# Optimization experiments

Measured on AMD Instinct MI355X. Metric: run time of the kernel, lower is better.

## Reference

```python
import jax, jax.numpy as jnp
import numpy as np

B, C, L, D, H = 8, 64, 256, 64, 4
HD = C // H  # head_dim = 16
EPS = 1e-5


def _conv(x, w):
    # x: [B,C,L,D], w: [O,I,kh,kw], stride 1, SAME padding (matches padding=1 for 3x3, 0 for 1x1)
    return jax.lax.conv_general_dilated(
        x, w, window_strides=(1, 1), padding='SAME',
        dimension_numbers=('NCHW', 'OIHW', 'NCHW'))


def setup_inputs() -> dict:
    rng = jax.random.key(0)
    ks = jax.random.split(rng, 10)
    n = lambda k, s: jax.random.normal(k, s, dtype=jnp.float32)
    xav3 = float(np.sqrt(6.0 / (C * 9 + C * 9)))  # xavier_uniform bound for 3x3 conv
    xav1 = float(np.sqrt(6.0 / (C + C)))
    u = lambda k, s, b: jax.random.uniform(k, s, jnp.float32, -b, b)
    return {
        'query': n(ks[0], (B, C, L, D)),
        'key': n(ks[1], (B, C, L, D)),
        'value': n(ks[2], (B, C, L, D)),
        'Wq': u(ks[3], (C, C, 3, 3), xav3),
        'Wk': u(ks[4], (C, C, 3, 3), xav3),
        'Wv': u(ks[5], (C, C, 3, 3), xav3),
        'Wo': u(ks[6], (C, C, 1, 1), xav1),
        'bo': jnp.zeros((C,), jnp.float32),
        'gamma': jnp.ones((C,), jnp.float32),
        'beta': jnp.zeros((C,), jnp.float32),
    }


def reference(query, key, value, Wq, Wk, Wv, Wo, bo, gamma, beta):
    identity = query
    # projections -> [B, H, HD, L, D]
    Q = _conv(query, Wq).reshape(B, H, HD, L, D)
    K = _conv(key, Wk).reshape(B, H, HD, L, D)
    V = _conv(value, Wv).reshape(B, H, HD, L, D)
    # attention over L, contraction over D; head_dim acts as an extra batch dim
    scores = jnp.einsum('bhcld,bhcmd->bhclm', Q, K) / jnp.sqrt(jnp.float32(HD))
    attn = jax.nn.softmax(scores, axis=-1)  # dropout is identity in eval mode
    out = jnp.einsum('bhclm,bhcmd->bhcld', attn, V).reshape(B, C, L, D)
    out = _conv(out, Wo) + bo[None, :, None, None] + identity
    # LayerNorm over channel dim (original permutes C last)
    mu = jnp.mean(out, axis=1, keepdims=True)
    var = jnp.var(out, axis=1, keepdims=True)
    out = (out - mu) * jax.lax.rsqrt(var + EPS)
    out = out * gamma[None, :, None, None] + beta[None, :, None, None]
    return out
```

## Files before the change

kernel.cpp:

```cpp
#include <hip/hip_runtime.h>

typedef _Float16 f16;
typedef f16   f16x8 __attribute__((ext_vector_type(8)));
typedef float f32x4 __attribute__((ext_vector_type(4)));

#define MFMA(a,b,c) __builtin_amdgcn_mfma_f32_16x16x32_f16(a,b,c,0,0,0)

__device__ __forceinline__ f32x4 fz4(){ f32x4 z; z[0]=0.f; z[1]=0.f; z[2]=0.f; z[3]=0.f; return z; }
__device__ __forceinline__ f16x8 hz8(){ f16x8 z;
#pragma unroll
  for(int i=0;i<8;++i) z[i]=(f16)0.f;
  return z; }

#define NBLK 256u

__device__ __forceinline__ void grid_barrier(unsigned* bar) {
  __syncthreads();
  if (threadIdx.x == 0) {
    __threadfence();
    unsigned gen  = atomicAdd(&bar[1], 0u);
    unsigned prev = atomicAdd(&bar[0], 1u);
    if (prev == NBLK - 1u) {
      atomicExch(&bar[0], 0u);
      __threadfence();
      atomicAdd(&bar[1], 1u);
    } else {
      while (atomicAdd(&bar[1], 0u) == gen) __builtin_amdgcn_s_sleep(2);
    }
    __threadfence();
  }
  __syncthreads();
}

__global__ __launch_bounds__(512, 2) void mega(
    const float* __restrict__ query, const float* __restrict__ key,
    const float* __restrict__ value,
    const float* __restrict__ Wq, const float* __restrict__ Wk,
    const float* __restrict__ Wv, const float* __restrict__ Wo,
    const float* __restrict__ bo, const float* __restrict__ gamma,
    const float* __restrict__ beta,
    f16* __restrict__ QKV, f16* __restrict__ AO,
    f16* WA, float* out, unsigned* bar)
{
  __shared__ f16 smem[32768];
  const int tid  = threadIdx.x;
  const int bid  = blockIdx.x;
  const int half = tid >> 8;
  const int ltid = tid & 255;
  const int lane = tid & 63;
  const int wvg  = tid >> 6;
  const int wvl  = (ltid >> 6);
  const int lr   = lane & 15, kh = lane >> 4;
  f16* hs = smem + half*16384;

  {
    int gid = bid*512 + tid;
    if (gid < 110592) {
      int t = gid / 36864, r = gid % 36864;
      const float* W = (t==0)?Wq:((t==1)?Wk:Wv);
      float sc = (t==0) ? 0.25f : 1.0f;
      int kstep = r >> 11, rem = r & 2047;
      int co = rem >> 5, rem2 = rem & 31;
      int kq = rem2 >> 3, j = rem2 & 7;
      int k = kstep*32 + kq*8 + j;
      int sp = k >> 6, ci = k & 63;
      int ky = sp/3, kx = sp - ky*3;
      WA[gid] = (f16)(W[((co*64+ci)*3+ky)*3+kx]*sc);
    }
  }
  grid_barrier(bar);

  for (int iter = 0; iter < 6; ++iter) {
    int w    = bid + (iter*2 + half)*256;
    int b    = w & 7;
    int rest = w >> 3;
    int t    = rest >> 7;
    int l0   = (rest & 127) * 2;
    const float* X = (t==0)?query:((t==1)?key:value);
    const f16* WAt = WA + t*36864;
    f16* Yt = QKV + (size_t)t*8388608;
    {
      int ci0 = (ltid & 31)*2;
      int row = (ltid >> 5) & 3;
      int dh  = (ltid >> 7) * 32;
      int gr  = l0 - 1 + row;
      bool valid = (unsigned)gr < 256u;
      int grc = valid ? gr : 0;
      const f32x4* s0 = (const f32x4*)(X + (((size_t)(b*64+ci0  )*256 + grc)*64 + dh));
      const f32x4* s1 = (const f32x4*)(X + (((size_t)(b*64+ci0+1)*256 + grc)*64 + dh));
#pragma unroll
      for (int q=0;q<8;++q) {
        f32x4 f0 = valid ? s0[q] : fz4();
        f32x4 f1 = valid ? s1[q] : fz4();
#pragma unroll
        for (int e=0;e<4;++e) {
          int d = dh + q*4 + e;
          int idx = ((row*64 + d)*64 + ci0) ^ ((d&7)<<3);
          unsigned int pk = (unsigned int)__builtin_bit_cast(unsigned short,(f16)f0[e])
                          | ((unsigned int)__builtin_bit_cast(unsigned short,(f16)f1[e]) << 16);
          *(unsigned int*)&hs[idx] = pk;
        }
      }
    }
    __syncthreads();
    f32x4 acc[4][2];
#pragma unroll
    for (int mt=0;mt<4;++mt){ acc[mt][0]=fz4(); acc[mt][1]=fz4(); }
    for (int kstep=0; kstep<18; ++kstep) {
      int sp = kstep >> 1;
      int sp3 = sp/3;
      int dl = sp3 - 1;
      int dd = (sp - sp3*3) - 1;
      int cib = (kstep & 1)*32;
      const f16* wp = WAt + kstep*2048 + lr*32 + kh*8;
      f16x8 a0 = *(const f16x8*)(wp);
      f16x8 a1 = *(const f16x8*)(wp + 512);
      f16x8 a2 = *(const f16x8*)(wp + 1024);
      f16x8 a3 = *(const f16x8*)(wp + 1536);
      f16x8 bb[2];
#pragma unroll
      for (int nt=0;nt<2;++nt) {
        int n = wvl*32 + nt*16 + lr;
        int lloc = n >> 6, d = n & 63;
        int dp = d + dd;
        bool v = (unsigned)dp < 64u;
        int dpc = dp & 63;
        int rowi = lloc + dl + 1;
        int idx = ((rowi*64 + dpc)*64 + cib + kh*8) ^ ((dpc&7)<<3);
        f16x8 tt = *(const f16x8*)&hs[idx];
        if (!v) tt = hz8();
        bb[nt] = tt;
      }
#pragma unroll
      for (int nt=0;nt<2;++nt) {
        acc[0][nt] = MFMA(a0, bb[nt], acc[0][nt]);
        acc[1][nt] = MFMA(a1, bb[nt], acc[1][nt]);
        acc[2][nt] = MFMA(a2, bb[nt], acc[2][nt]);
        acc[3][nt] = MFMA(a3, bb[nt], acc[3][nt]);
      }
    }
#pragma unroll
    for (int mt=0;mt<4;++mt)
#pragma unroll
    for (int nt=0;nt<2;++nt)
#pragma unroll
    for (int r=0;r<4;++r) {
      int co = mt*16 + kh*4 + r;
      int n = wvl*32 + nt*16 + lr;
      int lrow = l0 + (n>>6), d = n & 63;
      Yt[((size_t)(b*64+co)*256 + lrow)*64 + d] = (f16)acc[mt][nt][r];
    }
    __syncthreads();
  }
  grid_barrier(bar);

  for (int k2 = 0; k2 < 2; ++k2) {
    int idx = bid + k2*256;
    int bc = (idx & 7)*64 + (idx >> 3);
    const f16* Qs = QKV + (size_t)bc*16384;
    const f16* Ks = QKV +  8388608 + (size_t)bc*16384;
    const f16* Vs = QKV + 16777216 + (size_t)bc*16384;
    __syncthreads();
    {
      int m  = tid & 63;
      int dg = (tid >> 6) * 8;
#pragma unroll
      for (int pass=0; pass<4; ++pass) {
        int mm = m + pass*64;
        f16x8 v0 = *(const f16x8*)(Vs + mm*64 + dg);
#pragma unroll
        for (int e=0;e<8;++e){ int d=dg+e; smem[(d*256+mm) ^ ((d&7)<<3)] = v0[e]; }
      }
    }
    int l0g = wvg*32;
    f16x8 qf[2][2];
#pragma unroll
    for (int lt=0;lt<2;++lt)
#pragma unroll
    for (int ks=0;ks<2;++ks)
      qf[lt][ks] = *(const f16x8*)(Qs + (l0g + lt*16 + lr)*64 + ks*32 + kh*8);
    f32x4 O[2][4];
    float rm[2][4], rl[2][4];
#pragma unroll
    for (int lt=0;lt<2;++lt)
#pragma unroll
    for (int x=0;x<4;++x) { O[lt][x]=fz4(); rm[lt][x]=-1e30f; rl[lt][x]=0.f; }
    __syncthreads();
    f16* P = &smem[16384 + wvg*2048];
    for (int it=0; it<4; ++it) {
      int m0 = it*64;
      f32x4 s[2][4];
#pragma unroll
      for (int lt=0;lt<2;++lt)
#pragma unroll
      for (int mt=0;mt<4;++mt) s[lt][mt]=fz4();
#pragma unroll
      for (int ks=0;ks<2;++ks) {
        f16x8 kf[4];
#pragma unroll
        for (int mt=0;mt<4;++mt)
          kf[mt] = *(const f16x8*)(Ks + (m0 + mt*16 + lr)*64 + ks*32 + kh*8);
#pragma unroll
        for (int lt=0;lt<2;++lt)
#pragma unroll
        for (int mt=0;mt<4;++mt)
          s[lt][mt] = MFMA(qf[lt][ks], kf[mt], s[lt][mt]);
      }
#pragma unroll
      for (int lt=0;lt<2;++lt)
#pragma unroll
      for (int r=0;r<4;++r) {
        float tm = fmaxf(fmaxf(s[lt][0][r], s[lt][1][r]), fmaxf(s[lt][2][r], s[lt][3][r]));
#pragma unroll
        for (int off=1; off<16; off<<=1) tm = fmaxf(tm, __shfl_xor(tm, off));
        float mo = rm[lt][r];
        float mn = fmaxf(mo, tm);
        rm[lt][r] = mn;
        float corr = __expf(mo - mn);
        float sum = 0.f;
#pragma unroll
        for (int mt=0;mt<4;++mt) { float p = __expf(s[lt][mt][r] - mn); s[lt][mt][r] = p; sum += p; }
#pragma unroll
        for (int off=1; off<16; off<<=1) sum += __shfl_xor(sum, off);
        rl[lt][r] = rl[lt][r]*corr + sum;
#pragma unroll
        for (int dt=0;dt<4;++dt) O[lt][dt][r] *= corr;
      }
#pragma unroll
      for (int lt=0;lt<2;++lt)
#pragma unroll
      for (int mt=0;mt<4;++mt)
#pragma unroll
      for (int r=0;r<4;++r) {
        int row = lt*16 + kh*4 + r;
        P[(row*64 + mt*16 + lr) ^ ((row&7)<<3)] = (f16)s[lt][mt][r];
      }
#pragma unroll
      for (int ks=0;ks<2;++ks) {
        f16x8 pa[2], vb[4];
#pragma unroll
        for (int lt=0;lt<2;++lt) {
          int row = lt*16 + lr;
          pa[lt] = *(const f16x8*)&P[(row*64 + ks*32 + kh*8) ^ ((row&7)<<3)];
        }
#pragma unroll
        for (int dt=0;dt<4;++dt) {
          int d = dt*16 + lr;
          vb[dt] = *(const f16x8*)&smem[(d*256 + m0 + ks*32 + kh*8) ^ ((d&7)<<3)];
        }
#pragma unroll
        for (int lt=0;lt<2;++lt)
#pragma unroll
        for (int dt=0;dt<4;++dt)
          O[lt][dt] = MFMA(pa[lt], vb[dt], O[lt][dt]);
      }
    }
#pragma unroll
    for (int lt=0;lt<2;++lt)
#pragma unroll
    for (int r=0;r<4;++r) {
      float inv = 1.f / rl[lt][r];
      int row = l0g + lt*16 + kh*4 + r;
#pragma unroll
      for (int dt=0;dt<4;++dt)
        AO[(size_t)bc*16384 + row*64 + dt*16 + lr] = (f16)(O[lt][dt][r]*inv);
    }
  }
  grid_barrier(bar);

  for (int iter = 0; iter < 2; ++iter) {
    int w  = bid + (iter*2 + half)*256;
    int b  = w & 7;
    int p0 = (w >> 3) * 128;
    {
      int ci = ltid & 63;
      int pg = ltid >> 6;
      const f16* src = AO + (size_t)(b*64+ci)*16384 + p0 + pg*32;
      f16x8 v[4];
#pragma unroll
      for (int q=0;q<4;++q) v[q] = *(const f16x8*)(src + q*8);
#pragma unroll
      for (int q=0;q<4;++q)
#pragma unroll
      for (int e=0;e<8;++e) {
        int p = pg*32 + q*8 + e;
        hs[(p*64 + ci) ^ ((p&7)<<3)] = v[q][e];
      }
      int co  = ltid >> 2;
      int cig = (ltid & 3) * 16;
      const f32x4* wsrc = (const f32x4*)(Wo + co*64 + cig);
      f32x4 w0 = wsrc[0], w1 = wsrc[1], w2 = wsrc[2], w3 = wsrc[3];
      f16x8 g0, g1;
#pragma unroll
      for (int e=0;e<4;++e) { g0[e]=(f16)w0[e]; g0[4+e]=(f16)w1[e]; g1[e]=(f16)w2[e]; g1[4+e]=(f16)w3[e]; }
      *(f16x8*)&hs[8192 + ((co*64 + cig    ) ^ ((co&7)<<3))] = g0;
      *(f16x8*)&hs[8192 + ((co*64 + cig + 8) ^ ((co&7)<<3))] = g1;
    }
    __syncthreads();
    int n0 = wvl*32;
    f32x4 acc[4][2];
#pragma unroll
    for (int mt=0;mt<4;++mt){ acc[mt][0]=fz4(); acc[mt][1]=fz4(); }
#pragma unroll
    for (int ks=0;ks<2;++ks) {
      f16x8 a[4], bb[2];
#pragma unroll
      for (int mt=0;mt<4;++mt)
        a[mt] = *(const f16x8*)&hs[8192 + (((mt*16+lr)*64 + ks*32 + kh*8) ^ ((lr&7)<<3))];
#pragma unroll
      for (int nt=0;nt<2;++nt) {
        int p = n0 + nt*16 + lr;
        bb[nt] = *(const f16x8*)&hs[(p*64 + ks*32 + kh*8) ^ ((p&7)<<3)];
      }
#pragma unroll
      for (int mt=0;mt<4;++mt)
#pragma unroll
      for (int nt=0;nt<2;++nt)
        acc[mt][nt] = MFMA(a[mt], bb[nt], acc[mt][nt]);
    }
    float vals[4][2][4];
    float sum0=0.f, sq0=0.f, sum1=0.f, sq1=0.f;
#pragma unroll
    for (int mt=0;mt<4;++mt)
#pragma unroll
    for (int nt=0;nt<2;++nt)
#pragma unroll
    for (int r=0;r<4;++r) {
      int co = mt*16 + kh*4 + r;
      int p  = p0 + n0 + nt*16 + lr;
      float v = acc[mt][nt][r] + bo[co] + query[(size_t)(b*64+co)*16384 + p];
      vals[mt][nt][r] = v;
      if (nt==0) { sum0 += v; sq0 += v*v; } else { sum1 += v; sq1 += v*v; }
    }
#pragma unroll
    for (int off=16; off<64; off<<=1) {
      sum0 += __shfl_xor(sum0, off); sq0 += __shfl_xor(sq0, off);
      sum1 += __shfl_xor(sum1, off); sq1 += __shfl_xor(sq1, off);
    }
    float mu0 = sum0*(1.f/64.f), var0 = sq0*(1.f/64.f) - mu0*mu0, rs0 = rsqrtf(var0 + 1e-5f);
    float mu1 = sum1*(1.f/64.f), var1 = sq1*(1.f/64.f) - mu1*mu1, rs1 = rsqrtf(var1 + 1e-5f);
#pragma unroll
    for (int mt=0;mt<4;++mt)
#pragma unroll
    for (int nt=0;nt<2;++nt)
#pragma unroll
    for (int r=0;r<4;++r) {
      int co = mt*16 + kh*4 + r;
      int p  = p0 + n0 + nt*16 + lr;
      float mu = nt ? mu1 : mu0;
      float rs = nt ? rs1 : rs0;
      out[(size_t)(b*64+co)*16384 + p] = (vals[mt][nt][r] - mu)*rs*gamma[co] + beta[co];
    }
    __syncthreads();
  }
}

extern "C" void kernel_launch(void* const* d_in, const int* in_sizes, int n_in,
                              void* d_out, int out_size, void* d_ws, size_t ws_size,
                              hipStream_t stream)
{
  const float* query = (const float*)d_in[0];
  const float* key   = (const float*)d_in[1];
  const float* value = (const float*)d_in[2];
  const float* Wq = (const float*)d_in[3];
  const float* Wk = (const float*)d_in[4];
  const float* Wv = (const float*)d_in[5];
  const float* Wo = (const float*)d_in[6];
  const float* bo = (const float*)d_in[7];
  const float* gamma = (const float*)d_in[8];
  const float* beta  = (const float*)d_in[9];
  char* ws = (char*)d_ws;
  f16*      QKV  = (f16*)ws;
  f16*      AO   = (f16*)(ws + (size_t)50331648);
  f16*      WA   = (f16*)d_out;
  float*    outp = (float*)d_out;
  unsigned* bar  = (unsigned*)((char*)d_out + (size_t)(1<<20));

  hipMemsetAsync(bar, 0, 64, stream);
  mega<<<dim3(NBLK), dim3(512), 0, stream>>>(
      query, key, value, Wq, Wk, Wv, Wo, bo, gamma, beta,
      QKV, AO, WA, outp, bar);
}
```

Before: 238.8 us.

## Double block size to 1024 threads, halving per-wave work in every phase

Raises the persistent megakernel from 512 to 1024 threads per block and splits each phase's work across twice as many waves. Each wave now owns one 16-column MFMA tile instead of two in the conv, attention and output projection phases. The aim is more latency hiding and less register pressure per wave while keeping the 256-block grid barrier scheme. In exchange, each wave reuses loaded A-fragments (weights, K tiles) across fewer MFMAs, and a 1024-thread block limits how many blocks can sit on one CU.

Measured after the change: 292.0 us. +22.3%, slower.

```diff
diff --git a/kernel.cpp b/kernel.cpp
--- a/kernel.cpp
+++ b/kernel.cpp
@@ -32,7 +32,7 @@
   __syncthreads();
 }
 
-__global__ __launch_bounds__(512, 2) void mega(
+__global__ __launch_bounds__(1024) void mega(
     const float* __restrict__ query, const float* __restrict__ key,
     const float* __restrict__ value,
     const float* __restrict__ Wq, const float* __restrict__ Wk,
@@ -45,8 +45,8 @@
   __shared__ f16 smem[32768];
   const int tid  = threadIdx.x;
   const int bid  = blockIdx.x;
-  const int half = tid >> 8;
-  const int ltid = tid & 255;
+  const int half = tid >> 9;
+  const int ltid = tid & 511;
   const int lane = tid & 63;
   const int wvg  = tid >> 6;
   const int wvl  = (ltid >> 6);
@@ -54,7 +54,7 @@
   f16* hs = smem + half*16384;
 
   {
-    int gid = bid*512 + tid;
+    int gid = bid*1024 + tid;
     if (gid < 110592) {
       int t = gid / 36864, r = gid % 36864;
       const float* W = (t==0)?Wq:((t==1)?Wk:Wv);
@@ -82,14 +82,14 @@
     {
       int ci0 = (ltid & 31)*2;
       int row = (ltid >> 5) & 3;
-      int dh  = (ltid >> 7) * 32;
+      int dh  = (ltid >> 7) * 16;
       int gr  = l0 - 1 + row;
       bool valid = (unsigned)gr < 256u;
       int grc = valid ? gr : 0;
       const f32x4* s0 = (const f32x4*)(X + (((size_t)(b*64+ci0  )*256 + grc)*64 + dh));
       const f32x4* s1 = (const f32x4*)(X + (((size_t)(b*64+ci0+1)*256 + grc)*64 + dh));
 #pragma unroll
-      for (int q=0;q<8;++q) {
+      for (int q=0;q<4;++q) {
         f32x4 f0 = valid ? s0[q] : fz4();
         f32x4 f1 = valid ? s1[q] : fz4();
 #pragma unroll
@@ -103,9 +103,9 @@
       }
     }
     __syncthreads();
-    f32x4 acc[4][2];
-#pragma unroll
-    for (int mt=0;mt<4;++mt){ acc[mt][0]=fz4(); acc[mt][1]=fz4(); }
+    f32x4 acc[4];
+#pragma unroll
+    for (int mt=0;mt<4;++mt) acc[mt]=fz4();
     for (int kstep=0; kstep<18; ++kstep) {
       int sp = kstep >> 1;
       int sp3 = sp/3;
@@ -117,38 +117,31 @@
       f16x8 a1 = *(const f16x8*)(wp + 512);
       f16x8 a2 = *(const f16x8*)(wp + 1024);
       f16x8 a3 = *(const f16x8*)(wp + 1536);
-      f16x8 bb[2];
-#pragma unroll
-      for (int nt=0;nt<2;++nt) {
-        int n = wvl*32 + nt*16 + lr;
+      f16x8 bb;
+      {
+        int n = wvl*16 + lr;
         int lloc = n >> 6, d = n & 63;
         int dp = d + dd;
         bool v = (unsigned)dp < 64u;
         int dpc = dp & 63;
         int rowi = lloc + dl + 1;
         int idx = ((rowi*64 + dpc)*64 + cib + kh*8) ^ ((dpc&7)<<3);
-        f16x8 tt = *(const f16x8*)&hs[idx];
-        if (!v) tt = hz8();
-        bb[nt] = tt;
-      }
-#pragma unroll
-      for (int nt=0;nt<2;++nt) {
-        acc[0][nt] = MFMA(a0, bb[nt], acc[0][nt]);
-        acc[1][nt] = MFMA(a1, bb[nt], acc[1][nt]);
-        acc[2][nt] = MFMA(a2, bb[nt], acc[2][nt]);
-        acc[3][nt] = MFMA(a3, bb[nt], acc[3][nt]);
-      }
+        bb = *(const f16x8*)&hs[idx];
+        if (!v) bb = hz8();
+      }
+      acc[0] = MFMA(a0, bb, acc[0]);
+      acc[1] = MFMA(a1, bb, acc[1]);
+      acc[2] = MFMA(a2, bb, acc[2]);
+      acc[3] = MFMA(a3, bb, acc[3]);
     }
 #pragma unroll
     for (int mt=0;mt<4;++mt)
-#pragma unroll
-    for (int nt=0;nt<2;++nt)
 #pragma unroll
     for (int r=0;r<4;++r) {
       int co = mt*16 + kh*4 + r;
-      int n = wvl*32 + nt*16 + lr;
+      int n = wvl*16 + lr;
       int lrow = l0 + (n>>6), d = n & 63;
-      Yt[((size_t)(b*64+co)*256 + lrow)*64 + d] = (f16)acc[mt][nt][r];
+      Yt[((size_t)(b*64+co)*256 + lrow)*64 + d] = (f16)acc[mt][r];
     }
     __syncthreads();
   }
@@ -162,38 +155,31 @@
     const f16* Vs = QKV + 16777216 + (size_t)bc*16384;
     __syncthreads();
     {
-      int m  = tid & 63;
-      int dg = (tid >> 6) * 8;
-#pragma unroll
-      for (int pass=0; pass<4; ++pass) {
-        int mm = m + pass*64;
-        f16x8 v0 = *(const f16x8*)(Vs + mm*64 + dg);
-#pragma unroll
-        for (int e=0;e<8;++e){ int d=dg+e; smem[(d*256+mm) ^ ((d&7)<<3)] = v0[e]; }
-      }
-    }
-    int l0g = wvg*32;
-    f16x8 qf[2][2];
-#pragma unroll
-    for (int lt=0;lt<2;++lt)
+      int m  = tid & 255;
+      int dg = (tid >> 8) * 16;
+      f16x8 v0 = *(const f16x8*)(Vs + m*64 + dg);
+      f16x8 v1 = *(const f16x8*)(Vs + m*64 + dg + 8);
+#pragma unroll
+      for (int e=0;e<8;++e){ int d=dg+e;   smem[(d*256+m) ^ ((d&7)<<3)] = v0[e]; }
+#pragma unroll
+      for (int e=0;e<8;++e){ int d=dg+8+e; smem[(d*256+m) ^ ((d&7)<<3)] = v1[e]; }
+    }
+    int l0g = wvg*16;
+    f16x8 qf[2];
 #pragma unroll
     for (int ks=0;ks<2;++ks)
-      qf[lt][ks] = *(const f16x8*)(Qs + (l0g + lt*16 + lr)*64 + ks*32 + kh*8);
-    f32x4 O[2][4];
-    float rm[2][4], rl[2][4];
-#pragma unroll
-    for (int lt=0;lt<2;++lt)
-#pragma unroll
-    for (int x=0;x<4;++x) { O[lt][x]=fz4(); rm[lt][x]=-1e30f; rl[lt][x]=0.f; }
-    __syncthreads();
-    f16* P = &smem[16384 + wvg*2048];
+      qf[ks] = *(const f16x8*)(Qs + (l0g + lr)*64 + ks*32 + kh*8);
+    f32x4 O[4];
+    float rm[4], rl[4];
+#pragma unroll
+    for (int x=0;x<4;++x) { O[x]=fz4(); rm[x]=-1e30f; rl[x]=0.f; }
+    __syncthreads();
+    f16* P = &smem[16384 + wvg*1024];
     for (int it=0; it<4; ++it) {
       int m0 = it*64;
-      f32x4 s[2][4];
-#pragma unroll
-      for (int lt=0;lt<2;++lt)
-#pragma unroll
-      for (int mt=0;mt<4;++mt) s[lt][mt]=fz4();
+      f32x4 s[4];
+#pragma unroll
+      for (int mt=0;mt<4;++mt) s[mt]=fz4();
 #pragma unroll
       for (int ks=0;ks<2;++ks) {
         f16x8 kf[4];
@@ -201,47 +187,40 @@
         for (int mt=0;mt<4;++mt)
           kf[mt] = *(const f16x8*)(Ks + (m0 + mt*16 + lr)*64 + ks*32 + kh*8);
 #pragma unroll
-        for (int lt=0;lt<2;++lt)
-#pragma unroll
         for (int mt=0;mt<4;++mt)
-          s[lt][mt] = MFMA(qf[lt][ks], kf[mt], s[lt][mt]);
-      }
-#pragma unroll
-      for (int lt=0;lt<2;++lt)
+          s[mt] = MFMA(qf[ks], kf[mt], s[mt]);
+      }
 #pragma unroll
       for (int r=0;r<4;++r) {
-        float tm = fmaxf(fmaxf(s[lt][0][r], s[lt][1][r]), fmaxf(s[lt][2][r], s[lt][3][r]));
+        float tm = fmaxf(fmaxf(s[0][r], s[1][r]), fmaxf(s[2][r], s[3][r]));
 #pragma unroll
         for (int off=1; off<16; off<<=1) tm = fmaxf(tm, __shfl_xor(tm, off));
-        float mo = rm[lt][r];
+        float mo = rm[r];
         float mn = fmaxf(mo, tm);
-        rm[lt][r] = mn;
+        rm[r] = mn;
         float corr = __expf(mo - mn);
         float sum = 0.f;
 #pragma unroll
-        for (int mt=0;mt<4;++mt) { float p = __expf(s[lt][mt][r] - mn); s[lt][mt][r] = p; sum += p; }
+        for (int mt=0;mt<4;++mt) { float p = __expf(s[mt][r] - mn); s[mt][r] = p; sum += p; }
 #pragma unroll
         for (int off=1; off<16; off<<=1) sum += __shfl_xor(sum, off);
-        rl[lt][r] = rl[lt][r]*corr + sum;
-#pragma unroll
-        for (int dt=0;dt<4;++dt) O[lt][dt][r] *= corr;
-      }
-#pragma unroll
-      for (int lt=0;lt<2;++lt)
+        rl[r] = rl[r]*corr + sum;
+#pragma unroll
+        for (int dt=0;dt<4;++dt) O[dt][r] *= corr;
+      }
 #pragma unroll
       for (int mt=0;mt<4;++mt)
 #pragma unroll
       for (int r=0;r<4;++r) {
-        int row = lt*16 + kh*4 + r;
-        P[(row*64 + mt*16 + lr) ^ ((row&7)<<3)] = (f16)s[lt][mt][r];
+        int row = kh*4 + r;
+        P[(row*64 + mt*16 + lr) ^ ((row&7)<<3)] = (f16)s[mt][r];
       }
 #pragma unroll
       for (int ks=0;ks<2;++ks) {
-        f16x8 pa[2], vb[4];
-#pragma unroll
-        for (int lt=0;lt<2;++lt) {
-          int row = lt*16 + lr;
-          pa[lt] = *(const f16x8*)&P[(row*64 + ks*32 + kh*8) ^ ((row&7)<<3)];
+        f16x8 pa, vb[4];
+        {
+          int row = lr;
+          pa = *(const f16x8*)&P[(row*64 + ks*32 + kh*8) ^ ((row&7)<<3)];
         }
 #pragma unroll
         for (int dt=0;dt<4;++dt) {
@@ -249,21 +228,17 @@
           vb[dt] = *(const f16x8*)&smem[(d*256 + m0 + ks*32 + kh*8) ^ ((d&7)<<3)];
         }
 #pragma unroll
-        for (int lt=0;lt<2;++lt)
-#pragma unroll
         for (int dt=0;dt<4;++dt)
-          O[lt][dt] = MFMA(pa[lt], vb[dt], O[lt][dt]);
-      }
-    }
-#pragma unroll
-    for (int lt=0;lt<2;++lt)
+          O[dt] = MFMA(pa, vb[dt], O[dt]);
+      }
+    }
 #pragma unroll
     for (int r=0;r<4;++r) {
-      float inv = 1.f / rl[lt][r];
-      int row = l0g + lt*16 + kh*4 + r;
+      float inv = 1.f / rl[r];
+      int row = l0g + kh*4 + r;
 #pragma unroll
       for (int dt=0;dt<4;++dt)
-        AO[(size_t)bc*16384 + row*64 + dt*16 + lr] = (f16)(O[lt][dt][r]*inv);
+        AO[(size_t)bc*16384 + row*64 + dt*16 + lr] = (f16)(O[dt][r]*inv);
     }
   }
   grid_barrier(bar);
@@ -275,81 +250,71 @@
     {
       int ci = ltid & 63;
       int pg = ltid >> 6;
-      const f16* src = AO + (size_t)(b*64+ci)*16384 + p0 + pg*32;
-      f16x8 v[4];
-#pragma unroll
-      for (int q=0;q<4;++q) v[q] = *(const f16x8*)(src + q*8);
-#pragma unroll
-      for (int q=0;q<4;++q)
+      const f16* src = AO + (size_t)(b*64+ci)*16384 + p0 + pg*16;
+      f16x8 v0 = *(const f16x8*)(src);
+      f16x8 v1 = *(const f16x8*)(src + 8);
 #pragma unroll
       for (int e=0;e<8;++e) {
-        int p = pg*32 + q*8 + e;
-        hs[(p*64 + ci) ^ ((p&7)<<3)] = v[q][e];
-      }
-      int co  = ltid >> 2;
-      int cig = (ltid & 3) * 16;
+        int p = pg*16 + e;
+        hs[(p*64 + ci) ^ ((p&7)<<3)] = v0[e];
+      }
+#pragma unroll
+      for (int e=0;e<8;++e) {
+        int p = pg*16 + 8 + e;
+        hs[(p*64 + ci) ^ ((p&7)<<3)] = v1[e];
+      }
+      int co  = ltid >> 3;
+      int cig = (ltid & 7) * 8;
       const f32x4* wsrc = (const f32x4*)(Wo + co*64 + cig);
-      f32x4 w0 = wsrc[0], w1 = wsrc[1], w2 = wsrc[2], w3 = wsrc[3];
-      f16x8 g0, g1;
-#pragma unroll
-      for (int e=0;e<4;++e) { g0[e]=(f16)w0[e]; g0[4+e]=(f16)w1[e]; g1[e]=(f16)w2[e]; g1[4+e]=(f16)w3[e]; }
-      *(f16x8*)&hs[8192 + ((co*64 + cig    ) ^ ((co&7)<<3))] = g0;
-      *(f16x8*)&hs[8192 + ((co*64 + cig + 8) ^ ((co&7)<<3))] = g1;
-    }
-    __syncthreads();
-    int n0 = wvl*32;
-    f32x4 acc[4][2];
-#pragma unroll
-    for (int mt=0;mt<4;++mt){ acc[mt][0]=fz4(); acc[mt][1]=fz4(); }
+      f32x4 w0 = wsrc[0], w1 = wsrc[1];
+      f16x8 g0;
+#pragma unroll
+      for (int e=0;e<4;++e) { g0[e]=(f16)w0[e]; g0[4+e]=(f16)w1[e]; }
+      *(f16x8*)&hs[8192 + ((co*64 + cig) ^ ((co&7)<<3))] = g0;
+    }
+    __syncthreads();
+    int n0 = wvl*16;
+    f32x4 acc[4];
+#pragma unroll
+    for (int mt=0;mt<4;++mt) acc[mt]=fz4();
 #pragma unroll
     for (int ks=0;ks<2;++ks) {
-      f16x8 a[4], bb[2];
+      f16x8 a[4], bb;
 #pragma unroll
       for (int mt=0;mt<4;++mt)
         a[mt] = *(const f16x8*)&hs[8192 + (((mt*16+lr)*64 + ks*32 + kh*8) ^ ((lr&7)<<3))];
-#pragma unroll
-      for (int nt=0;nt<2;++nt) {
-        int p = n0 + nt*16 + lr;
-        bb[nt] = *(const f16x8*)&hs[(p*64 + ks*32 + kh*8) ^ ((p&7)<<3)];
+      {
+        int p = n0 + lr;
+        bb = *(const f16x8*)&hs[(p*64 + ks*32 + kh*8) ^ ((p&7)<<3)];
       }
 #pragma unroll
       for (int mt=0;mt<4;++mt)
-#pragma unroll
-      for (int nt=0;nt<2;++nt)
-        acc[mt][nt] = MFMA(a[mt], bb[nt], acc[mt][nt]);
-    }
-    float vals[4][2][4];
-    float sum0=0.f, sq0=0.f, sum1=0.f, sq1=0.f;
+        acc[mt] = MFMA(a[mt], bb, acc[mt]);
+    }
+    float vals[4][4];
+    float sum0=0.f, sq0=0.f;
 #pragma unroll
     for (int mt=0;mt<4;++mt)
-#pragma unroll
-    for (int nt=0;nt<2;++nt)
 #pragma unroll
     for (int r=0;r<4;++r) {
       int co = mt*16 + kh*4 + r;
-      int p  = p0 + n0 + nt*16 + lr;
-      float v = acc[mt][nt][r] + bo[co] + query[(size_t)(b*64+co)*16384 + p];
-      vals[mt][nt][r] = v;
-      if (nt==0) { sum0 += v; sq0 += v*v; } else { sum1 += v; sq1 += v*v; }
+      int p  = p0 + n0 + lr;
+      float v = acc[mt][r] + bo[co] + query[(size_t)(b*64+co)*16384 + p];
+      vals[mt][r] = v;
+      sum0 += v; sq0 += v*v;
     }
 #pragma unroll
     for (int off=16; off<64; off<<=1) {
       sum0 += __shfl_xor(sum0, off); sq0 += __shfl_xor(sq0, off);
-      sum1 += __shfl_xor(sum1, off); sq1 += __shfl_xor(sq1, off);
     }
     float mu0 = sum0*(1.f/64.f), var0 = sq0*(1.f/64.f) - mu0*mu0, rs0 = rsqrtf(var0 + 1e-5f);
-    float mu1 = sum1*(1.f/64.f), var1 = sq1*(1.f/64.f) - mu1*mu1, rs1 = rsqrtf(var1 + 1e-5f);
 #pragma unroll
     for (int mt=0;mt<4;++mt)
-#pragma unroll
-    for (int nt=0;nt<2;++nt)
 #pragma unroll
     for (int r=0;r<4;++r) {
       int co = mt*16 + kh*4 + r;
-      int p  = p0 + n0 + nt*16 + lr;
-      float mu = nt ? mu1 : mu0;
-      float rs = nt ? rs1 : rs0;
-      out[(size_t)(b*64+co)*16384 + p] = (vals[mt][nt][r] - mu)*rs*gamma[co] + beta[co];
+      int p  = p0 + n0 + lr;
+      out[(size_t)(b*64+co)*16384 + p] = (vals[mt][r] - mu0)*rs0*gamma[co] + beta[co];
     }
     __syncthreads();
   }
@@ -377,7 +342,7 @@
   unsigned* bar  = (unsigned*)((char*)d_out + (size_t)(1<<20));
 
   hipMemsetAsync(bar, 0, 64, stream);
-  mega<<<dim3(NBLK), dim3(512), 0, stream>>>(
+  mega<<<dim3(NBLK), dim3(1024), 0, stream>>>(
       query, key, value, Wq, Wk, Wv, Wo, bo, gamma, beta,
       QKV, AO, WA, outp, bar);
 }
```

## Double persistent block size to 1024 threads and re-split all phases

Applied to the files above, without the earlier changes.

Launches the persistent grid-barrier kernel with 1024 threads per block instead of 512 and doubles shared memory. The conv phase now runs four work quarters per block over three iterations, and the output-projection phase runs in a single pass. In attention, each wave now handles 16 query rows instead of 32. The aim is to put twice as many waves on each CU, since only 256 blocks exist and each CU previously held one 8-wave block, to hide latency better. The trade-off is less register-level reuse per wave in attention, plus a larger LDS footprint and more block-wide synchronisation cost.

After: 290.9 us. 21.8% more time.

```diff
diff --git a/kernel.cpp b/kernel.cpp
--- a/kernel.cpp
+++ b/kernel.cpp
@@ -32,7 +32,7 @@
   __syncthreads();
 }
 
-__global__ __launch_bounds__(512, 2) void mega(
+__global__ __launch_bounds__(1024) void mega(
     const float* __restrict__ query, const float* __restrict__ key,
     const float* __restrict__ value,
     const float* __restrict__ Wq, const float* __restrict__ Wk,
@@ -42,19 +42,19 @@
     f16* __restrict__ QKV, f16* __restrict__ AO,
     f16* WA, float* out, unsigned* bar)
 {
-  __shared__ f16 smem[32768];
+  __shared__ f16 smem[65536];
   const int tid  = threadIdx.x;
   const int bid  = blockIdx.x;
-  const int half = tid >> 8;
+  const int q4   = tid >> 8;
   const int ltid = tid & 255;
   const int lane = tid & 63;
   const int wvg  = tid >> 6;
   const int wvl  = (ltid >> 6);
   const int lr   = lane & 15, kh = lane >> 4;
-  f16* hs = smem + half*16384;
+  f16* hs = smem + q4*16384;
 
   {
-    int gid = bid*512 + tid;
+    int gid = bid*1024 + tid;
     if (gid < 110592) {
       int t = gid / 36864, r = gid % 36864;
       const float* W = (t==0)?Wq:((t==1)?Wk:Wv);
@@ -70,8 +70,8 @@
   }
   grid_barrier(bar);
 
-  for (int iter = 0; iter < 6; ++iter) {
-    int w    = bid + (iter*2 + half)*256;
+  for (int iter = 0; iter < 3; ++iter) {
+    int w    = bid + (iter*4 + q4)*256;
     int b    = w & 7;
     int rest = w >> 3;
     int t    = rest >> 7;
@@ -162,38 +162,31 @@
     const f16* Vs = QKV + 16777216 + (size_t)bc*16384;
     __syncthreads();
     {
-      int m  = tid & 63;
-      int dg = (tid >> 6) * 8;
-#pragma unroll
-      for (int pass=0; pass<4; ++pass) {
-        int mm = m + pass*64;
-        f16x8 v0 = *(const f16x8*)(Vs + mm*64 + dg);
-#pragma unroll
-        for (int e=0;e<8;++e){ int d=dg+e; smem[(d*256+mm) ^ ((d&7)<<3)] = v0[e]; }
-      }
-    }
-    int l0g = wvg*32;
-    f16x8 qf[2][2];
-#pragma unroll
-    for (int lt=0;lt<2;++lt)
+      int m  = tid & 255;
+      int dg = (tid >> 8) * 16;
+      f16x8 v0 = *(const f16x8*)(Vs + m*64 + dg);
+      f16x8 v1 = *(const f16x8*)(Vs + m*64 + dg + 8);
+#pragma unroll
+      for (int e=0;e<8;++e){ int d=dg+e;   smem[(d*256+m) ^ ((d&7)<<3)] = v0[e]; }
+#pragma unroll
+      for (int e=0;e<8;++e){ int d=dg+8+e; smem[(d*256+m) ^ ((d&7)<<3)] = v1[e]; }
+    }
+    int l0g = wvg*16;
+    f16x8 qf[2];
 #pragma unroll
     for (int ks=0;ks<2;++ks)
-      qf[lt][ks] = *(const f16x8*)(Qs + (l0g + lt*16 + lr)*64 + ks*32 + kh*8);
-    f32x4 O[2][4];
-    float rm[2][4], rl[2][4];
-#pragma unroll
-    for (int lt=0;lt<2;++lt)
-#pragma unroll
-    for (int x=0;x<4;++x) { O[lt][x]=fz4(); rm[lt][x]=-1e30f; rl[lt][x]=0.f; }
-    __syncthreads();
-    f16* P = &smem[16384 + wvg*2048];
+      qf[ks] = *(const f16x8*)(Qs + (l0g + lr)*64 + ks*32 + kh*8);
+    f32x4 O[4];
+    float rm[4], rl[4];
+#pragma unroll
+    for (int x=0;x<4;++x) { O[x]=fz4(); rm[x]=-1e30f; rl[x]=0.f; }
+    __syncthreads();
+    f16* P = &smem[16384 + wvg*1024];
     for (int it=0; it<4; ++it) {
       int m0 = it*64;
-      f32x4 s[2][4];
-#pragma unroll
-      for (int lt=0;lt<2;++lt)
-#pragma unroll
-      for (int mt=0;mt<4;++mt) s[lt][mt]=fz4();
+      f32x4 s[4];
+#pragma unroll
+      for (int mt=0;mt<4;++mt) s[mt]=fz4();
 #pragma unroll
       for (int ks=0;ks<2;++ks) {
         f16x8 kf[4];
@@ -201,47 +194,40 @@
         for (int mt=0;mt<4;++mt)
           kf[mt] = *(const f16x8*)(Ks + (m0 + mt*16 + lr)*64 + ks*32 + kh*8);
 #pragma unroll
-        for (int lt=0;lt<2;++lt)
-#pragma unroll
         for (int mt=0;mt<4;++mt)
-          s[lt][mt] = MFMA(qf[lt][ks], kf[mt], s[lt][mt]);
-      }
-#pragma unroll
-      for (int lt=0;lt<2;++lt)
+          s[mt] = MFMA(qf[ks], kf[mt], s[mt]);
+      }
 #pragma unroll
       for (int r=0;r<4;++r) {
-        float tm = fmaxf(fmaxf(s[lt][0][r], s[lt][1][r]), fmaxf(s[lt][2][r], s[lt][3][r]));
+        float tm = fmaxf(fmaxf(s[0][r], s[1][r]), fmaxf(s[2][r], s[3][r]));
 #pragma unroll
         for (int off=1; off<16; off<<=1) tm = fmaxf(tm, __shfl_xor(tm, off));
-        float mo = rm[lt][r];
+        float mo = rm[r];
         float mn = fmaxf(mo, tm);
-        rm[lt][r] = mn;
+        rm[r] = mn;
         float corr = __expf(mo - mn);
         float sum = 0.f;
 #pragma unroll
-        for (int mt=0;mt<4;++mt) { float p = __expf(s[lt][mt][r] - mn); s[lt][mt][r] = p; sum += p; }
+        for (int mt=0;mt<4;++mt) { float p = __expf(s[mt][r] - mn); s[mt][r] = p; sum += p; }
 #pragma unroll
         for (int off=1; off<16; off<<=1) sum += __shfl_xor(sum, off);
-        rl[lt][r] = rl[lt][r]*corr + sum;
-#pragma unroll
-        for (int dt=0;dt<4;++dt) O[lt][dt][r] *= corr;
-      }
-#pragma unroll
-      for (int lt=0;lt<2;++lt)
+        rl[r] = rl[r]*corr + sum;
+#pragma unroll
+        for (int dt=0;dt<4;++dt) O[dt][r] *= corr;
+      }
 #pragma unroll
       for (int mt=0;mt<4;++mt)
 #pragma unroll
       for (int r=0;r<4;++r) {
-        int row = lt*16 + kh*4 + r;
-        P[(row*64 + mt*16 + lr) ^ ((row&7)<<3)] = (f16)s[lt][mt][r];
+        int row = kh*4 + r;
+        P[(row*64 + mt*16 + lr) ^ ((row&7)<<3)] = (f16)s[mt][r];
       }
 #pragma unroll
       for (int ks=0;ks<2;++ks) {
-        f16x8 pa[2], vb[4];
-#pragma unroll
-        for (int lt=0;lt<2;++lt) {
-          int row = lt*16 + lr;
-          pa[lt] = *(const f16x8*)&P[(row*64 + ks*32 + kh*8) ^ ((row&7)<<3)];
+        f16x8 pa, vb[4];
+        {
+          int row = lr;
+          pa = *(const f16x8*)&P[(row*64 + ks*32 + kh*8) ^ ((row&7)<<3)];
         }
 #pragma unroll
         for (int dt=0;dt<4;++dt) {
@@ -249,27 +235,23 @@
           vb[dt] = *(const f16x8*)&smem[(d*256 + m0 + ks*32 + kh*8) ^ ((d&7)<<3)];
         }
 #pragma unroll
-        for (int lt=0;lt<2;++lt)
-#pragma unroll
         for (int dt=0;dt<4;++dt)
-          O[lt][dt] = MFMA(pa[lt], vb[dt], O[lt][dt]);
-      }
-    }
-#pragma unroll
-    for (int lt=0;lt<2;++lt)
+          O[dt] = MFMA(pa, vb[dt], O[dt]);
+      }
+    }
 #pragma unroll
     for (int r=0;r<4;++r) {
-      float inv = 1.f / rl[lt][r];
-      int row = l0g + lt*16 + kh*4 + r;
+      float inv = 1.f / rl[r];
+      int row = l0g + kh*4 + r;
 #pragma unroll
       for (int dt=0;dt<4;++dt)
-        AO[(size_t)bc*16384 + row*64 + dt*16 + lr] = (f16)(O[lt][dt][r]*inv);
+        AO[(size_t)bc*16384 + row*64 + dt*16 + lr] = (f16)(O[dt][r]*inv);
     }
   }
   grid_barrier(bar);
 
-  for (int iter = 0; iter < 2; ++iter) {
-    int w  = bid + (iter*2 + half)*256;
+  {
+    int w  = bid + q4*256;
     int b  = w & 7;
     int p0 = (w >> 3) * 128;
     {
@@ -351,7 +333,6 @@
       float rs = nt ? rs1 : rs0;
       out[(size_t)(b*64+co)*16384 + p] = (vals[mt][nt][r] - mu)*rs*gamma[co] + beta[co];
     }
-    __syncthreads();
   }
 }
 
@@ -377,7 +358,7 @@
   unsigned* bar  = (unsigned*)((char*)d_out + (size_t)(1<<20));
 
   hipMemsetAsync(bar, 0, 64, stream);
-  mega<<<dim3(NBLK), dim3(512), 0, stream>>>(
+  mega<<<dim3(NBLK), dim3(1024), 0, stream>>>(
       query, key, value, Wq, Wk, Wv, Wo, bo, gamma, beta,
       QKV, AO, WA, outp, bar);
 }
```

## Double-buffer conv input tiles and prefetch next weight slice in conv phase

Applied to the files above, without the earlier changes.

The projection-conv phase now prefetches the next iteration's fp32 input rows into registers while the current tile's MFMAs run, then writes them into a second LDS buffer (shared memory doubled to 128 KB). Weight fragments for the next k-step are also loaded one step ahead. The aim is to hide global-load latency behind compute. In exchange, register pressure rises (64 extra fp32 registers per thread) and the larger LDS footprint may reduce the 2-blocks-per-CU occupancy assumed by the launch bounds.

After: 294.2 us. 1.23x slower.

```diff
diff --git a/kernel.cpp b/kernel.cpp
--- a/kernel.cpp
+++ b/kernel.cpp
@@ -42,7 +42,7 @@
     f16* __restrict__ QKV, f16* __restrict__ AO,
     f16* WA, float* out, unsigned* bar)
 {
-  __shared__ f16 smem[32768];
+  __shared__ f16 smem[65536];
   const int tid  = threadIdx.x;
   const int bid  = blockIdx.x;
   const int half = tid >> 8;
@@ -70,19 +70,23 @@
   }
   grid_barrier(bar);
 
-  for (int iter = 0; iter < 6; ++iter) {
-    int w    = bid + (iter*2 + half)*256;
-    int b    = w & 7;
-    int rest = w >> 3;
-    int t    = rest >> 7;
-    int l0   = (rest & 127) * 2;
-    const float* X = (t==0)?query:((t==1)?key:value);
-    const f16* WAt = WA + t*36864;
-    f16* Yt = QKV + (size_t)t*8388608;
-    {
-      int ci0 = (ltid & 31)*2;
-      int row = (ltid >> 5) & 3;
-      int dh  = (ltid >> 7) * 32;
+  {
+    f16* bufA = smem + half*16384;
+    f16* bufB = smem + 32768 + half*16384;
+    const int ci0 = (ltid & 31)*2;
+    const int row = (ltid >> 5) & 3;
+    const int dh  = (ltid >> 7) * 32;
+
+    f32x4 r0[8], r1[8];
+    int ct=0, cl0=0, cb=0;
+
+    auto conv_load = [&](int iter, int& t_o, int& l0_o, int& b_o) {
+      int w    = bid + (iter*2 + half)*256;
+      int b    = w & 7;
+      int rest = w >> 3;
+      int t    = rest >> 7;
+      int l0   = (rest & 127) * 2;
+      const float* X = (t==0)?query:((t==1)?key:value);
       int gr  = l0 - 1 + row;
       bool valid = (unsigned)gr < 256u;
       int grc = valid ? gr : 0;
@@ -90,67 +94,100 @@
       const f32x4* s1 = (const f32x4*)(X + (((size_t)(b*64+ci0+1)*256 + grc)*64 + dh));
 #pragma unroll
       for (int q=0;q<8;++q) {
-        f32x4 f0 = valid ? s0[q] : fz4();
-        f32x4 f1 = valid ? s1[q] : fz4();
-#pragma unroll
-        for (int e=0;e<4;++e) {
-          int d = dh + q*4 + e;
-          int idx = ((row*64 + d)*64 + ci0) ^ ((d&7)<<3);
-          unsigned int pk = (unsigned int)__builtin_bit_cast(unsigned short,(f16)f0[e])
-                          | ((unsigned int)__builtin_bit_cast(unsigned short,(f16)f1[e]) << 16);
-          *(unsigned int*)&hs[idx] = pk;
+        r0[q] = valid ? s0[q] : fz4();
+        r1[q] = valid ? s1[q] : fz4();
+      }
+      t_o = t; l0_o = l0; b_o = b;
+    };
+
+    auto conv_write = [&](f16* buf) {
+#pragma unroll
+      for (int q=0;q<8;++q)
+#pragma unroll
+      for (int e=0;e<4;++e) {
+        int d = dh + q*4 + e;
+        int idx = ((row*64 + d)*64 + ci0) ^ ((d&7)<<3);
+        unsigned int pk = (unsigned int)__builtin_bit_cast(unsigned short,(f16)r0[q][e])
+                        | ((unsigned int)__builtin_bit_cast(unsigned short,(f16)r1[q][e]) << 16);
+        *(unsigned int*)&buf[idx] = pk;
+      }
+    };
+
+    auto conv_compute = [&](const f16* buf, int t, int l0, int b) {
+      const f16* WAt = WA + t*36864;
+      f16* Yt = QKV + (size_t)t*8388608;
+      f32x4 acc[4][2];
+#pragma unroll
+      for (int mt=0;mt<4;++mt){ acc[mt][0]=fz4(); acc[mt][1]=fz4(); }
+      const f16* wbase = WAt + lr*32 + kh*8;
+      f16x8 a0 = *(const f16x8*)(wbase);
+      f16x8 a1 = *(const f16x8*)(wbase + 512);
+      f16x8 a2 = *(const f16x8*)(wbase + 1024);
+      f16x8 a3 = *(const f16x8*)(wbase + 1536);
+      for (int kstep=0; kstep<18; ++kstep) {
+        f16x8 n0, n1, n2, n3;
+        if (kstep < 17) {
+          const f16* wp = wbase + (kstep+1)*2048;
+          n0 = *(const f16x8*)(wp);
+          n1 = *(const f16x8*)(wp + 512);
+          n2 = *(const f16x8*)(wp + 1024);
+          n3 = *(const f16x8*)(wp + 1536);
         }
-      }
-    }
+        int sp = kstep >> 1;
+        int sp3 = sp/3;
+        int dl = sp3 - 1;
+        int dd = (sp - sp3*3) - 1;
+        int cib = (kstep & 1)*32;
+        f16x8 bb[2];
+#pragma unroll
+        for (int nt=0;nt<2;++nt) {
+          int n = wvl*32 + nt*16 + lr;
+          int lloc = n >> 6, d = n & 63;
+          int dp = d + dd;
+          bool v = (unsigned)dp < 64u;
+          int dpc = dp & 63;
+          int rowi = lloc + dl + 1;
+          int idx = ((rowi*64 + dpc)*64 + cib + kh*8) ^ ((dpc&7)<<3);
+          f16x8 tt = *(const f16x8*)&buf[idx];
+          if (!v) tt = hz8();
+          bb[nt] = tt;
+        }
+#pragma unroll
+        for (int nt=0;nt<2;++nt) {
+          acc[0][nt] = MFMA(a0, bb[nt], acc[0][nt]);
+          acc[1][nt] = MFMA(a1, bb[nt], acc[1][nt]);
+          acc[2][nt] = MFMA(a2, bb[nt], acc[2][nt]);
+          acc[3][nt] = MFMA(a3, bb[nt], acc[3][nt]);
+        }
+        a0 = n0; a1 = n1; a2 = n2; a3 = n3;
+      }
+#pragma unroll
+      for (int mt=0;mt<4;++mt)
+#pragma unroll
+      for (int nt=0;nt<2;++nt)
+#pragma unroll
+      for (int r=0;r<4;++r) {
+        int co = mt*16 + kh*4 + r;
+        int n = wvl*32 + nt*16 + lr;
+        int lrow = l0 + (n>>6), d = n & 63;
+        Yt[((size_t)(b*64+co)*256 + lrow)*64 + d] = (f16)acc[mt][nt][r];
+      }
+    };
+
+    conv_load(0, ct, cl0, cb);
+    conv_write(bufA);
     __syncthreads();
-    f32x4 acc[4][2];
-#pragma unroll
-    for (int mt=0;mt<4;++mt){ acc[mt][0]=fz4(); acc[mt][1]=fz4(); }
-    for (int kstep=0; kstep<18; ++kstep) {
-      int sp = kstep >> 1;
-      int sp3 = sp/3;
-      int dl = sp3 - 1;
-      int dd = (sp - sp3*3) - 1;
-      int cib = (kstep & 1)*32;
-      const f16* wp = WAt + kstep*2048 + lr*32 + kh*8;
-      f16x8 a0 = *(const f16x8*)(wp);
-      f16x8 a1 = *(const f16x8*)(wp + 512);
-      f16x8 a2 = *(const f16x8*)(wp + 1024);
-      f16x8 a3 = *(const f16x8*)(wp + 1536);
-      f16x8 bb[2];
-#pragma unroll
-      for (int nt=0;nt<2;++nt) {
-        int n = wvl*32 + nt*16 + lr;
-        int lloc = n >> 6, d = n & 63;
-        int dp = d + dd;
-        bool v = (unsigned)dp < 64u;
-        int dpc = dp & 63;
-        int rowi = lloc + dl + 1;
-        int idx = ((rowi*64 + dpc)*64 + cib + kh*8) ^ ((dpc&7)<<3);
-        f16x8 tt = *(const f16x8*)&hs[idx];
-        if (!v) tt = hz8();
-        bb[nt] = tt;
-      }
-#pragma unroll
-      for (int nt=0;nt<2;++nt) {
-        acc[0][nt] = MFMA(a0, bb[nt], acc[0][nt]);
-        acc[1][nt] = MFMA(a1, bb[nt], acc[1][nt]);
-        acc[2][nt] = MFMA(a2, bb[nt], acc[2][nt]);
-        acc[3][nt] = MFMA(a3, bb[nt], acc[3][nt]);
-      }
-    }
-#pragma unroll
-    for (int mt=0;mt<4;++mt)
-#pragma unroll
-    for (int nt=0;nt<2;++nt)
-#pragma unroll
-    for (int r=0;r<4;++r) {
-      int co = mt*16 + kh*4 + r;
-      int n = wvl*32 + nt*16 + lr;
-      int lrow = l0 + (n>>6), d = n & 63;
-      Yt[((size_t)(b*64+co)*256 + lrow)*64 + d] = (f16)acc[mt][nt][r];
-    }
-    __syncthreads();
+    for (int iter = 0; iter < 6; ++iter) {
+      int nt_=0, nl0=0, nb=0;
+      if (iter < 5) conv_load(iter+1, nt_, nl0, nb);
+      conv_compute((iter & 1) ? bufB : bufA, ct, cl0, cb);
+      if (iter < 5) {
+        __syncthreads();
+        conv_write((iter & 1) ? bufA : bufB);
+        __syncthreads();
+        ct = nt_; cl0 = nl0; cb = nb;
+      }
+    }
   }
   grid_barrier(bar);
 
```
